# Optimization experiments

Hardware: AMD Instinct MI355X
Metric: run time of the kernel (lower is better)

## Reference

```python
import jax, jax.numpy as jnp
import numpy as np

D = 128      # d_single
DP = 64      # d_pair
H = 8        # nhead
DH = D // H  # head dim = 16
DO = 32      # outer proj dim


def layernorm(x, g, b, eps=1e-5):
    mu = jnp.mean(x, axis=-1, keepdims=True)
    var = jnp.var(x, axis=-1, keepdims=True)
    return (x - mu) * jax.lax.rsqrt(var + eps) * g + b


def setup_inputs() -> dict:
    key = jax.random.key(0)
    ks = jax.random.split(key, 16)
    B, L = 2, 320
    s = 0.02
    return {
        "x": jax.random.normal(ks[0], (B, L, D), jnp.float32),
        "z": jax.random.normal(ks[1], (B, L, L, DP), jnp.float32),
        "Wq": jax.random.normal(ks[2], (D, D), jnp.float32) * s,
        "Wk": jax.random.normal(ks[3], (D, D), jnp.float32) * s,
        "Wv": jax.random.normal(ks[4], (D, D), jnp.float32) * s,
        "Wb": jax.random.normal(ks[5], (DP, H), jnp.float32) * s,
        "Wo": jax.random.normal(ks[6], (D, D), jnp.float32) * s,
        "bo": jnp.zeros((D,), jnp.float32),
        "ln1_g": jnp.ones((D,), jnp.float32),
        "ln1_b": jnp.zeros((D,), jnp.float32),
        "W_ffn1": jax.random.normal(ks[7], (D, 4 * D), jnp.float32) * s,
        "b_ffn1": jnp.zeros((4 * D,), jnp.float32),
        "W_ffn2": jax.random.normal(ks[8], (4 * D, D), jnp.float32) * s,
        "b_ffn2": jnp.zeros((D,), jnp.float32),
        "ln2_g": jnp.ones((D,), jnp.float32),
        "ln2_b": jnp.zeros((D,), jnp.float32),
        "Wp1": jax.random.normal(ks[9], (D, DO), jnp.float32) * s,
        "bp1": jnp.zeros((DO,), jnp.float32),
        "Wp2": jax.random.normal(ks[10], (D, DO), jnp.float32) * s,
        "bp2": jnp.zeros((DO,), jnp.float32),
        "Wz": jax.random.normal(ks[11], (DO * DO, DP), jnp.float32) * s,
        "bz": jnp.zeros((DP,), jnp.float32),
        "lnp_g": jnp.ones((DP,), jnp.float32),
        "lnp_b": jnp.zeros((DP,), jnp.float32),
    }


def reference(x, z, Wq, Wk, Wv, Wb, Wo, bo, ln1_g, ln1_b,
              W_ffn1, b_ffn1, W_ffn2, b_ffn2, ln2_g, ln2_b,
              Wp1, bp1, Wp2, bp2, Wz, bz, lnp_g, lnp_b):
    B, L, _ = x.shape
    # --- pair-biased self-attention (dropout = identity in eval) ---
    xn = layernorm(x, ln1_g, ln1_b)
    q = (xn @ Wq).reshape(B, L, H, DH)
    k = (xn @ Wk).reshape(B, L, H, DH)
    v = (xn @ Wv).reshape(B, L, H, DH)
    bias = jnp.einsum('bijp,ph->bhij', z, Wb)                 # [B,H,L,L]
    scores = jnp.einsum('bihd,bjhd->bhij', q, k) / jnp.sqrt(jnp.float32(DH))
    probs = jax.nn.softmax(scores + bias, axis=-1)
    out = jnp.einsum('bhij,bjhd->bihd', probs, v).reshape(B, L, D)
    x = x + out @ Wo + bo
    # --- FFN ---
    xn2 = layernorm(x, ln2_g, ln2_b)
    h = jax.nn.gelu(xn2 @ W_ffn1 + b_ffn1, approximate=False)
    x = x + h @ W_ffn2 + b_ffn2
    # --- outer-product pair update ---
    p1 = x @ Wp1 + bp1                                        # [B,L,32]
    p2 = x @ Wp2 + bp2                                        # [B,L,32]
    # einsum('bic,bjd->bijcd') then flatten(-2) then GEMM with Wz
    Wz4 = Wz.reshape(DO, DO, DP)
    upd = jnp.einsum('bic,bjd,cdp->bijp', p1, p2, Wz4) + bz   # [B,L,L,DP]
    z = layernorm(z + upd, lnp_g, lnp_b)
    return (x, z)
```

## Files before the change

kernel.cpp:

```cpp
#include <hip/hip_runtime.h>
#include <math.h>

#define D   128
#define DP  64
#define H   8
#define DH  16
#define DO  32
#define NB  2
#define L   320
#define NR  (NB * L)

typedef float f4 __attribute__((ext_vector_type(4)));

__global__ __launch_bounds__(256) void k1_ln_qkv(
    const float* __restrict__ x, const float* __restrict__ Wq,
    const float* __restrict__ Wk, const float* __restrict__ Wv,
    const float* __restrict__ g, const float* __restrict__ bb,
    float* __restrict__ qkv) {
  __shared__ float xs[2][D];
  __shared__ float stat[2][2];
  const int t = threadIdx.x;
  const int r0 = blockIdx.x * 2;
  const int row = t >> 7, c = t & 127;
  xs[row][c] = x[(r0 + row) * D + c];
  __syncthreads();
  const int w = t >> 6, lane = t & 63;
  if (w < 2) {
    float a = xs[w][lane], cc = xs[w][lane + 64];
    float s = a + cc, s2 = a * a + cc * cc;
#pragma unroll
    for (int off = 32; off >= 1; off >>= 1) {
      s += __shfl_xor(s, off, 64);
      s2 += __shfl_xor(s2, off, 64);
    }
    if (lane == 0) {
      float mu = s * (1.0f / D);
      float var = s2 * (1.0f / D) - mu * mu;
      stat[w][0] = mu;
      stat[w][1] = rsqrtf(var + 1e-5f);
    }
  }
  __syncthreads();
  float xn = (xs[row][c] - stat[row][0]) * stat[row][1] * g[c] + bb[c];
  xs[row][c] = xn;
  __syncthreads();
  float aq = 0, ak = 0, av = 0;
#pragma unroll 4
  for (int k = 0; k < D; ++k) {
    float wq = Wq[k * D + c], wk = Wk[k * D + c], wv = Wv[k * D + c];
    float xv = xs[row][k];
    aq += xv * wq;
    ak += xv * wk;
    av += xv * wv;
  }
  int base = (r0 + row) * 384 + c;
  qkv[base] = aq;
  qkv[base + 128] = ak;
  qkv[base + 256] = av;
}

__global__ __launch_bounds__(256) void k2_bias(
    const float* __restrict__ z, const float* __restrict__ Wb,
    float* __restrict__ bias) {
  __shared__ float zs[64][65];
  __shared__ float wbs[DP * H];
  const int t = threadIdx.x;
  const int jt = blockIdx.x, i = blockIdx.y, b = blockIdx.z;
  const f4* zsrc4 =
      (const f4*)(z + (((size_t)(b * L + i) * L) + jt * 64) * DP);
#pragma unroll
  for (int q = 0; q < 4; ++q) {
    int idx4 = q * 256 + t;
    f4 v = zsrc4[idx4];
    int r = idx4 >> 4, c0 = (idx4 & 15) * 4;
    zs[r][c0] = v.x; zs[r][c0 + 1] = v.y; zs[r][c0 + 2] = v.z; zs[r][c0 + 3] = v.w;
  }
  for (int q = t; q < DP * H; q += 256) wbs[q] = Wb[q];
  __syncthreads();
  const int h0 = t >> 6, j = t & 63;
  float a0 = 0, a1 = 0;
#pragma unroll 8
  for (int p = 0; p < 64; ++p) {
    float zv = zs[j][p];
    a0 += zv * wbs[p * H + h0];
    a1 += zv * wbs[p * H + h0 + 4];
  }
  size_t o0 = (((size_t)(b * H + h0) * L) + i) * L + jt * 64 + j;
  bias[o0] = a0;
  bias[o0 + (size_t)4 * L * L] = a1;
}

__global__ __launch_bounds__(1024, 8) void k3_attn(
    const float* __restrict__ qkv, const float* __restrict__ bias,
    float* __restrict__ ao) {
  __shared__ float Ks[L * 17];
  __shared__ float Vs[L * 17];
  __shared__ float qs[16 * DH];
  __shared__ float ps[16][L];
  const int t = threadIdx.x;
  const int i0 = blockIdx.x * 16, h = blockIdx.y, b = blockIdx.z;
  for (int idx = t; idx < L * DH; idx += 1024) {
    int j = idx >> 4, d = idx & 15;
    const float* src = qkv + (size_t)(b * L + j) * 384 + h * DH + d;
    Ks[j * 17 + d] = src[128];
    Vs[j * 17 + d] = src[256];
  }
  if (t < 256) {
    int ii = t >> 4, d = t & 15;
    qs[t] = qkv[(size_t)(b * L + i0 + ii) * 384 + h * DH + d] * 0.25f;
  }
  __syncthreads();
  const int w = t >> 6, lane = t & 63;
  const int i = i0 + w;
  const float* brow = bias + (((size_t)(b * H + h) * L) + i) * L;
  float sc[5], m = -1e30f;
#pragma unroll
  for (int it = 0; it < 5; ++it) {
    int j = it * 64 + lane;
    float s = 0;
#pragma unroll
    for (int d = 0; d < DH; ++d) s += qs[w * DH + d] * Ks[j * 17 + d];
    s += brow[j];
    sc[it] = s;
    m = fmaxf(m, s);
  }
#pragma unroll
  for (int off = 32; off >= 1; off >>= 1) m = fmaxf(m, __shfl_xor(m, off, 64));
  float sum = 0;
#pragma unroll
  for (int it = 0; it < 5; ++it) {
    sc[it] = __expf(sc[it] - m);
    sum += sc[it];
  }
#pragma unroll
  for (int off = 32; off >= 1; off >>= 1) sum += __shfl_xor(sum, off, 64);
  float inv = 1.0f / sum;
#pragma unroll
  for (int it = 0; it < 5; ++it) ps[w][it * 64 + lane] = sc[it];
  int d = lane & 15, grp = lane >> 4;
  float acc = 0;
#pragma unroll 4
  for (int j = grp * 80; j < grp * 80 + 80; ++j) acc += ps[w][j] * Vs[j * 17 + d];
  acc += __shfl_xor(acc, 16, 64);
  acc += __shfl_xor(acc, 32, 64);
  if (lane < 16) ao[(size_t)(b * L + i) * D + h * DH + d] = acc * inv;
}

__global__ __launch_bounds__(512, 4) void k45_rowpass(
    const float* __restrict__ x, const float* __restrict__ ao,
    const float* __restrict__ Wo, const float* __restrict__ bo,
    const float* __restrict__ g2, const float* __restrict__ b2,
    const float* __restrict__ W1, const float* __restrict__ bf1,
    const float* __restrict__ W2, const float* __restrict__ bf2,
    const float* __restrict__ Wp1, const float* __restrict__ bp1,
    const float* __restrict__ Wp2, const float* __restrict__ bp2,
    const float* __restrict__ Wz,
    float* __restrict__ out_x, float* __restrict__ p1, float* __restrict__ p2,
    float* __restrict__ T) {
  __shared__ float aos[2][D];
  __shared__ float x1s[2][D];
  __shared__ float nrm[2][D];
  __shared__ float x2s[2][D];
  __shared__ float hs[2][512];
  __shared__ __align__(16) float redbuf[4096];
  __shared__ float ps_row[2][64];
  __shared__ float stat[2][2];
  f4* red4 = (f4*)redbuf;
  const int t = threadIdx.x;
  const int r0 = blockIdx.x * 2;
  if (t < 256) { int r = t >> 7, c = t & 127; aos[r][c] = ao[(r0 + r) * D + c]; }
  __syncthreads();
  {
    int cg = t & 31, q = t >> 5;
    f4 a0 = {0, 0, 0, 0}, a1 = {0, 0, 0, 0};
#pragma unroll
    for (int k = q * 8; k < q * 8 + 8; ++k) {
      f4 wv = ((const f4*)(Wo + k * D))[cg];
      float v0 = aos[0][k], v1 = aos[1][k];
      a0 += v0 * wv;
      a1 += v1 * wv;
    }
    red4[(q * 2 + 0) * 32 + cg] = a0;
    red4[(q * 2 + 1) * 32 + cg] = a1;
  }
  __syncthreads();
  if (t < 256) {
    int r = t >> 7, c = t & 127;
    float a = x[(r0 + r) * D + c] + bo[c];
#pragma unroll
    for (int q = 0; q < 16; ++q) a += redbuf[q * 256 + r * 128 + c];
    x1s[r][c] = a;
  }
  __syncthreads();
  if (t < 128) {
    int w = t >> 6, lane = t & 63;
    float a = x1s[w][lane], cc = x1s[w][lane + 64];
    float s = a + cc, s2 = a * a + cc * cc;
#pragma unroll
    for (int off = 32; off >= 1; off >>= 1) {
      s += __shfl_xor(s, off, 64);
      s2 += __shfl_xor(s2, off, 64);
    }
    if (lane == 0) {
      float mu = s * (1.0f / D);
      stat[w][0] = mu;
      stat[w][1] = rsqrtf(s2 * (1.0f / D) - mu * mu + 1e-5f);
    }
  }
  __syncthreads();
  if (t < 256) {
    int r = t >> 7, c = t & 127;
    nrm[r][c] = (x1s[r][c] - stat[r][0]) * stat[r][1] * g2[c] + b2[c];
  }
  __syncthreads();
  {
    int cg = t & 127, q = t >> 7;
    f4 a0 = {0, 0, 0, 0}, a1 = {0, 0, 0, 0};
#pragma unroll 4
    for (int k = q * 32; k < q * 32 + 32; ++k) {
      f4 wv = ((const f4*)(W1 + k * 512))[cg];
      float v0 = nrm[0][k], v1 = nrm[1][k];
      a0 += v0 * wv;
      a1 += v1 * wv;
    }
    red4[q * 256 + 0 * 128 + cg] = a0;
    red4[q * 256 + 1 * 128 + cg] = a1;
  }
  __syncthreads();
  {
#pragma unroll
    for (int r = 0; r < 2; ++r) {
      float a = bf1[t];
#pragma unroll
      for (int q = 0; q < 4; ++q) a += redbuf[q * 1024 + r * 512 + t];
      hs[r][t] = 0.5f * a * (1.0f + erff(a * 0.70710678118654752f));
    }
  }
  __syncthreads();
  {
    int cg = t & 31, q = t >> 5;
    f4 a0 = {0, 0, 0, 0}, a1 = {0, 0, 0, 0};
#pragma unroll 4
    for (int k = q * 32; k < q * 32 + 32; ++k) {
      f4 wv = ((const f4*)(W2 + k * D))[cg];
      float v0 = hs[0][k], v1 = hs[1][k];
      a0 += v0 * wv;
      a1 += v1 * wv;
    }
    red4[(q * 2 + 0) * 32 + cg] = a0;
    red4[(q * 2 + 1) * 32 + cg] = a1;
  }
  __syncthreads();
  if (t < 256) {
    int r = t >> 7, c = t & 127;
    float a = x1s[r][c] + bf2[c];
#pragma unroll
    for (int q = 0; q < 16; ++q) a += redbuf[q * 256 + r * 128 + c];
    x2s[r][c] = a;
    out_x[(r0 + r) * D + c] = a;
  }
  __syncthreads();
  {
    int o = t & 63, r = (t >> 6) & 1, q = t >> 7;
    const float* W = (o < 32) ? Wp1 : Wp2;
    int cc = o & 31;
    float a = 0;
#pragma unroll
    for (int k = q * 32; k < q * 32 + 32; ++k) a += x2s[r][k] * W[k * DO + cc];
    redbuf[t] = a;
  }
  __syncthreads();
  if (t < 128) {
    int r = t >> 6, o = t & 63;
    float a = redbuf[0 * 128 + r * 64 + o] + redbuf[1 * 128 + r * 64 + o] +
              redbuf[2 * 128 + r * 64 + o] + redbuf[3 * 128 + r * 64 + o] +
              ((o < 32) ? bp1[o] : bp2[o & 31]);
    ps_row[r][o] = a;
    if (o < 32) p1[(r0 + r) * DO + o] = a;
    else        p2[(r0 + r) * DO + (o & 31)] = a;
  }
  __syncthreads();
  {
    const f4* Wz4 = (const f4*)Wz;
    f4 a0 = {0, 0, 0, 0}, a1 = {0, 0, 0, 0};
#pragma unroll 8
    for (int cc = 0; cc < 32; ++cc) {
      f4 wv = Wz4[cc * 512 + t];
      float v0 = ps_row[0][cc], v1 = ps_row[1][cc];
      a0 += v0 * wv;
      a1 += v1 * wv;
    }
    ((f4*)T)[(size_t)(r0 + 0) * 512 + t] = a0;
    ((f4*)T)[(size_t)(r0 + 1) * 512 + t] = a1;
  }
}

__global__ __launch_bounds__(256) void k6_zout(
    const float* __restrict__ z, const float* __restrict__ T,
    const float* __restrict__ p2, const float* __restrict__ bz,
    const float* __restrict__ gp, const float* __restrict__ bp,
    float* __restrict__ zout) {
  __shared__ __align__(16) f4 tds[32][16];
  __shared__ __align__(16) float p2s[80 * DO];
  const int t = threadIdx.x;
  const int jt = blockIdx.x;
  const int i = blockIdx.y, b = blockIdx.z;
  const size_t row = (size_t)(b * L + i);
  {
    const f4* Tsrc = (const f4*)(T + row * 2048);
    f4* tflat = (f4*)tds;
    tflat[t] = Tsrc[t];
    tflat[t + 256] = Tsrc[t + 256];
    const f4* psrc4 = (const f4*)(p2 + ((size_t)b * L + jt * 80) * DO);
    f4* p2s4 = (f4*)p2s;
    for (int q = t; q < 640; q += 256) p2s4[q] = psrc4[q];
  }
  const int w = t >> 6, lane = t & 63;
  const int jj = lane >> 4, pq = lane & 15;
  const f4 bz4 = ((const f4*)bz)[pq];
  const f4 g4 = ((const f4*)gp)[pq];
  const f4 b4 = ((const f4*)bp)[pq];
  __syncthreads();
  const float* zbase = z + (row * L + (size_t)jt * 80) * DP;
  float* obase = zout + (row * L + (size_t)jt * 80) * DP;
#pragma unroll
  for (int q = 0; q < 5; ++q) {
    const int jl = w * 20 + q * 4 + jj;
    f4 zv = ((const f4*)(zbase + jl * DP))[pq];
    f4 acc0 = bz4, acc1 = {0, 0, 0, 0};
#pragma unroll
    for (int d = 0; d < 32; d += 2) {
      acc0 += p2s[jl * DO + d] * tds[d][pq];
      acc1 += p2s[jl * DO + d + 1] * tds[d + 1][pq];
    }
    f4 y = zv + acc0 + acc1;
    float s = y.x + y.y + y.z + y.w;
    float s2 = y.x * y.x + y.y * y.y + y.z * y.z + y.w * y.w;
#pragma unroll
    for (int off = 8; off >= 1; off >>= 1) {
      s += __shfl_xor(s, off, 64);
      s2 += __shfl_xor(s2, off, 64);
    }
    float mu = s * (1.0f / DP);
    float var = s2 * (1.0f / DP) - mu * mu;
    float r = rsqrtf(var + 1e-5f);
    f4 out = (y - mu) * r * g4 + b4;
    ((f4*)(obase + jl * DP))[pq] = out;
  }
}

extern "C" void kernel_launch(void* const* d_in, const int* in_sizes, int n_in,
                              void* d_out, int out_size, void* d_ws, size_t ws_size,
                              hipStream_t stream) {
  const float* x      = (const float*)d_in[0];
  const float* z      = (const float*)d_in[1];
  const float* Wq     = (const float*)d_in[2];
  const float* Wk     = (const float*)d_in[3];
  const float* Wv     = (const float*)d_in[4];
  const float* Wb     = (const float*)d_in[5];
  const float* Wo     = (const float*)d_in[6];
  const float* bo     = (const float*)d_in[7];
  const float* ln1_g  = (const float*)d_in[8];
  const float* ln1_b  = (const float*)d_in[9];
  const float* W_ffn1 = (const float*)d_in[10];
  const float* b_ffn1 = (const float*)d_in[11];
  const float* W_ffn2 = (const float*)d_in[12];
  const float* b_ffn2 = (const float*)d_in[13];
  const float* ln2_g  = (const float*)d_in[14];
  const float* ln2_b  = (const float*)d_in[15];
  const float* Wp1    = (const float*)d_in[16];
  const float* bp1    = (const float*)d_in[17];
  const float* Wp2    = (const float*)d_in[18];
  const float* bp2    = (const float*)d_in[19];
  const float* Wz     = (const float*)d_in[20];
  const float* bz     = (const float*)d_in[21];
  const float* lnp_g  = (const float*)d_in[22];
  const float* lnp_b  = (const float*)d_in[23];

  float* ws   = (float*)d_ws;
  float* qkv  = ws;
  float* bias = qkv + 245760;
  float* ao   = bias + 1638400;
  float* p1   = ao + 81920;
  float* p2   = p1 + 20480;
  float* T    = p2 + 20480;

  float* out_x = (float*)d_out;
  float* out_z = out_x + 81920;

  hipLaunchKernelGGL(k1_ln_qkv, dim3(NR / 2), dim3(256), 0, stream,
                     x, Wq, Wk, Wv, ln1_g, ln1_b, qkv);
  hipLaunchKernelGGL(k2_bias, dim3(L / 64, L, NB), dim3(256), 0, stream,
                     z, Wb, bias);
  hipLaunchKernelGGL(k3_attn, dim3(L / 16, H, NB), dim3(1024), 0, stream,
                     qkv, bias, ao);
  hipLaunchKernelGGL(k45_rowpass, dim3(NR / 2), dim3(512), 0, stream,
                     x, ao, Wo, bo, ln2_g, ln2_b, W_ffn1, b_ffn1,
                     W_ffn2, b_ffn2, Wp1, bp1, Wp2, bp2, Wz, out_x, p1, p2, T);
  hipLaunchKernelGGL(k6_zout, dim3(4, L, NB), dim3(256), 0, stream,
                     z, T, p2, bz, lnp_g, lnp_b, out_z);
}
```

Measured before the change: 207.8 us.

## Merge LN/QKV and pair-bias kernels into one launch; shrink attention blocks

The LayerNorm+QKV projection kernel and the z→bias projection kernel become a single launch. Blocks below 320 do the QKV rows and the rest do bias tiles, removing one kernel boundary and letting the two independent jobs overlap. The attention kernel moves from 1024-thread blocks covering 16 query rows to 256-thread blocks covering 4 rows, with vectorized float4 loads of K/V into shared memory. This should improve occupancy and scheduling flexibility, but each K/V tile is now reloaded by four times as many blocks.

After: 204.0 us. Within noise of the previous version (-1.8%).

```diff
diff --git a/kernel.cpp b/kernel.cpp
--- a/kernel.cpp
+++ b/kernel.cpp
@@ -12,100 +12,106 @@
 
 typedef float f4 __attribute__((ext_vector_type(4)));
 
-__global__ __launch_bounds__(256) void k1_ln_qkv(
+__global__ __launch_bounds__(256) void k12_qkv_bias(
     const float* __restrict__ x, const float* __restrict__ Wq,
     const float* __restrict__ Wk, const float* __restrict__ Wv,
     const float* __restrict__ g, const float* __restrict__ bb,
-    float* __restrict__ qkv) {
-  __shared__ float xs[2][D];
-  __shared__ float stat[2][2];
-  const int t = threadIdx.x;
-  const int r0 = blockIdx.x * 2;
-  const int row = t >> 7, c = t & 127;
-  xs[row][c] = x[(r0 + row) * D + c];
-  __syncthreads();
-  const int w = t >> 6, lane = t & 63;
-  if (w < 2) {
-    float a = xs[w][lane], cc = xs[w][lane + 64];
-    float s = a + cc, s2 = a * a + cc * cc;
-#pragma unroll
-    for (int off = 32; off >= 1; off >>= 1) {
-      s += __shfl_xor(s, off, 64);
-      s2 += __shfl_xor(s2, off, 64);
-    }
-    if (lane == 0) {
-      float mu = s * (1.0f / D);
-      float var = s2 * (1.0f / D) - mu * mu;
-      stat[w][0] = mu;
-      stat[w][1] = rsqrtf(var + 1e-5f);
-    }
-  }
-  __syncthreads();
-  float xn = (xs[row][c] - stat[row][0]) * stat[row][1] * g[c] + bb[c];
-  xs[row][c] = xn;
-  __syncthreads();
-  float aq = 0, ak = 0, av = 0;
-#pragma unroll 4
-  for (int k = 0; k < D; ++k) {
-    float wq = Wq[k * D + c], wk = Wk[k * D + c], wv = Wv[k * D + c];
-    float xv = xs[row][k];
-    aq += xv * wq;
-    ak += xv * wk;
-    av += xv * wv;
-  }
-  int base = (r0 + row) * 384 + c;
-  qkv[base] = aq;
-  qkv[base + 128] = ak;
-  qkv[base + 256] = av;
-}
-
-__global__ __launch_bounds__(256) void k2_bias(
+    float* __restrict__ qkv,
     const float* __restrict__ z, const float* __restrict__ Wb,
     float* __restrict__ bias) {
   __shared__ float zs[64][65];
   __shared__ float wbs[DP * H];
   const int t = threadIdx.x;
-  const int jt = blockIdx.x, i = blockIdx.y, b = blockIdx.z;
-  const f4* zsrc4 =
-      (const f4*)(z + (((size_t)(b * L + i) * L) + jt * 64) * DP);
-#pragma unroll
-  for (int q = 0; q < 4; ++q) {
-    int idx4 = q * 256 + t;
-    f4 v = zsrc4[idx4];
-    int r = idx4 >> 4, c0 = (idx4 & 15) * 4;
-    zs[r][c0] = v.x; zs[r][c0 + 1] = v.y; zs[r][c0 + 2] = v.z; zs[r][c0 + 3] = v.w;
-  }
-  for (int q = t; q < DP * H; q += 256) wbs[q] = Wb[q];
-  __syncthreads();
-  const int h0 = t >> 6, j = t & 63;
-  float a0 = 0, a1 = 0;
+  if (blockIdx.x < 320) {
+    float* xs = &zs[0][0];
+    float* stat = &wbs[0];
+    const int r0 = blockIdx.x * 2;
+    const int row = t >> 7, c = t & 127;
+    xs[row * D + c] = x[(r0 + row) * D + c];
+    __syncthreads();
+    const int w = t >> 6, lane = t & 63;
+    if (w < 2) {
+      float a = xs[w * D + lane], cc = xs[w * D + lane + 64];
+      float s = a + cc, s2 = a * a + cc * cc;
+#pragma unroll
+      for (int off = 32; off >= 1; off >>= 1) {
+        s += __shfl_xor(s, off, 64);
+        s2 += __shfl_xor(s2, off, 64);
+      }
+      if (lane == 0) {
+        float mu = s * (1.0f / D);
+        float var = s2 * (1.0f / D) - mu * mu;
+        stat[w * 2 + 0] = mu;
+        stat[w * 2 + 1] = rsqrtf(var + 1e-5f);
+      }
+    }
+    __syncthreads();
+    float xn = (xs[row * D + c] - stat[row * 2]) * stat[row * 2 + 1] * g[c] + bb[c];
+    __syncthreads();
+    xs[row * D + c] = xn;
+    __syncthreads();
+    float aq = 0, ak = 0, av = 0;
+#pragma unroll 4
+    for (int k = 0; k < D; ++k) {
+      float wq = Wq[k * D + c], wk = Wk[k * D + c], wv = Wv[k * D + c];
+      float xv = xs[row * D + k];
+      aq += xv * wq;
+      ak += xv * wk;
+      av += xv * wv;
+    }
+    int base = (r0 + row) * 384 + c;
+    qkv[base] = aq;
+    qkv[base + 128] = ak;
+    qkv[base + 256] = av;
+  } else {
+    const int bi = blockIdx.x - 320;
+    const int jt = bi % 5;
+    const int i = (bi / 5) % L;
+    const int b = bi / (5 * L);
+    const f4* zsrc4 =
+        (const f4*)(z + (((size_t)(b * L + i) * L) + jt * 64) * DP);
+#pragma unroll
+    for (int q = 0; q < 4; ++q) {
+      int idx4 = q * 256 + t;
+      f4 v = zsrc4[idx4];
+      int r = idx4 >> 4, c0 = (idx4 & 15) * 4;
+      zs[r][c0] = v.x; zs[r][c0 + 1] = v.y; zs[r][c0 + 2] = v.z; zs[r][c0 + 3] = v.w;
+    }
+    for (int q = t; q < DP * H; q += 256) wbs[q] = Wb[q];
+    __syncthreads();
+    const int h0 = t >> 6, j = t & 63;
+    float a0 = 0, a1 = 0;
 #pragma unroll 8
-  for (int p = 0; p < 64; ++p) {
-    float zv = zs[j][p];
-    a0 += zv * wbs[p * H + h0];
-    a1 += zv * wbs[p * H + h0 + 4];
-  }
-  size_t o0 = (((size_t)(b * H + h0) * L) + i) * L + jt * 64 + j;
-  bias[o0] = a0;
-  bias[o0 + (size_t)4 * L * L] = a1;
+    for (int p = 0; p < 64; ++p) {
+      float zv = zs[j][p];
+      a0 += zv * wbs[p * H + h0];
+      a1 += zv * wbs[p * H + h0 + 4];
+    }
+    size_t o0 = (((size_t)(b * H + h0) * L) + i) * L + jt * 64 + j;
+    bias[o0] = a0;
+    bias[o0 + (size_t)4 * L * L] = a1;
+  }
 }
 
-__global__ __launch_bounds__(1024, 8) void k3_attn(
+__global__ __launch_bounds__(256) void k3_attn(
     const float* __restrict__ qkv, const float* __restrict__ bias,
     float* __restrict__ ao) {
   __shared__ float Ks[L * 17];
   __shared__ float Vs[L * 17];
-  __shared__ float qs[16 * DH];
-  __shared__ float ps[16][L];
+  __shared__ float qs[4 * DH];
+  __shared__ float ps[4][L];
   const int t = threadIdx.x;
-  const int i0 = blockIdx.x * 16, h = blockIdx.y, b = blockIdx.z;
-  for (int idx = t; idx < L * DH; idx += 1024) {
-    int j = idx >> 4, d = idx & 15;
-    const float* src = qkv + (size_t)(b * L + j) * 384 + h * DH + d;
-    Ks[j * 17 + d] = src[128];
-    Vs[j * 17 + d] = src[256];
-  }
-  if (t < 256) {
+  const int i0 = blockIdx.x * 4, h = blockIdx.y, b = blockIdx.z;
+  const f4* qkv4 = (const f4*)qkv;
+  for (int idx = t; idx < 2560; idx += 256) {
+    int isV = idx >= 1280;
+    int e = idx - isV * 1280;
+    int j = e >> 2, sub = e & 3;
+    f4 v = qkv4[(size_t)(b * L + j) * 96 + h * 4 + (isV ? 64 : 32) + sub];
+    float* dst = (isV ? Vs : Ks) + j * 17 + sub * 4;
+    dst[0] = v.x; dst[1] = v.y; dst[2] = v.z; dst[3] = v.w;
+  }
+  if (t < 64) {
     int ii = t >> 4, d = t & 15;
     qs[t] = qkv[(size_t)(b * L + i0 + ii) * 384 + h * DH + d] * 0.25f;
   }
@@ -388,11 +394,9 @@
   float* out_x = (float*)d_out;
   float* out_z = out_x + 81920;
 
-  hipLaunchKernelGGL(k1_ln_qkv, dim3(NR / 2), dim3(256), 0, stream,
-                     x, Wq, Wk, Wv, ln1_g, ln1_b, qkv);
-  hipLaunchKernelGGL(k2_bias, dim3(L / 64, L, NB), dim3(256), 0, stream,
-                     z, Wb, bias);
-  hipLaunchKernelGGL(k3_attn, dim3(L / 16, H, NB), dim3(1024), 0, stream,
+  hipLaunchKernelGGL(k12_qkv_bias, dim3(320 + 5 * L * NB), dim3(256), 0, stream,
+                     x, Wq, Wk, Wv, ln1_g, ln1_b, qkv, z, Wb, bias);
+  hipLaunchKernelGGL(k3_attn, dim3(L / 4, H, NB), dim3(256), 0, stream,
                      qkv, bias, ao);
   hipLaunchKernelGGL(k45_rowpass, dim3(NR / 2), dim3(512), 0, stream,
                      x, ao, Wo, bo, ln2_g, ln2_b, W_ffn1, b_ffn1,
```
